# Performance work log

Measured on AMD Instinct MI355X. Metric: run time of the kernel, lower is better.

Reference implementation:

```python
import jax, jax.numpy as jnp
import numpy as np

IN_CH, OUT_CH = 32, 32
MODES1, MODES2 = 16, 16
B, H, W = 16, 256, 256


def setup_inputs() -> dict:
    key = jax.random.key(0)
    k1, k2, k3 = jax.random.split(key, 3)
    scale = 1.0 / (IN_CH * OUT_CH)
    x = jax.random.normal(k1, (B, IN_CH, H, W), dtype=jnp.float32)
    # weights stored as real view of complex: [..., 2] = (real, imag)
    w1 = scale * jax.random.uniform(k2, (IN_CH, OUT_CH, MODES1, MODES2, 2), dtype=jnp.float32)
    w2 = scale * jax.random.uniform(k3, (IN_CH, OUT_CH, MODES1, MODES2, 2), dtype=jnp.float32)
    return {"x": x, "w1": w1, "w2": w2}


def reference(x, w1, w2):
    m1, m2 = MODES1, MODES2
    b, _, h, w = x.shape
    x_ft = jnp.fft.rfft2(x, axes=(-2, -1))  # [B, in_ch, H, W//2+1] complex
    c1 = w1[..., 0] + 1j * w1[..., 1]       # [in_ch, out_ch, m1, m2]
    c2 = w2[..., 0] + 1j * w2[..., 1]
    o1 = jnp.einsum('bixy,ioxy->boxy', x_ft[:, :, :m1, :m2], c1)
    o2 = jnp.einsum('bixy,ioxy->boxy', x_ft[:, :, -m1:, :m2], c2)
    out_ft = jnp.zeros((b, c1.shape[1], h, w // 2 + 1), dtype=x_ft.dtype)
    out_ft = out_ft.at[:, :, :m1, :m2].set(o1)
    out_ft = out_ft.at[:, :, -m1:, :m2].set(o2)
    return jnp.fft.irfft2(out_ft, s=(h, w), axes=(-2, -1))
```

## Files before the change

### kernel.cpp

```cpp
#include <hip/hip_runtime.h>
#include <math.h>

#define BB 16
#define CC 32
#define HH 256
#define WW 256
#define NIMG (BB * CC)

typedef _Float16 f16;
typedef __attribute__((ext_vector_type(8))) _Float16 f16x8;
typedef __attribute__((ext_vector_type(4))) float f32x4;

constexpr float TWO_PI_OVER_256 = 6.28318530717958647692f / 256.0f;

#define N_TWF 8192
#define N_ACOL 32768
#define N_AINV 16384
#define N_BINV 8192

static __device__ __forceinline__ f32x4 mfma3(f16x8 ah, f16x8 al, f16x8 bh,
                                              f16x8 bl, f32x4 c) {
  c = __builtin_amdgcn_mfma_f32_16x16x32_f16(ah, bh, c, 0, 0, 0);
  c = __builtin_amdgcn_mfma_f32_16x16x32_f16(ah, bl, c, 0, 0, 0);
  c = __builtin_amdgcn_mfma_f32_16x16x32_f16(al, bh, c, 0, 0, 0);
  return c;
}

static __device__ __forceinline__ void split16(float v, f16* hi, f16* lo) {
  f16 h_ = (f16)v;
  *hi = h_;
  *lo = (f16)(v - (float)h_);
}

__global__ __launch_bounds__(256) void k_tw(f16* __restrict__ fb) {
  const int id = blockIdx.x * 256 + threadIdx.x;
  f16* twf_hi = fb;
  f16* twf_lo = twf_hi + N_TWF;
  f16* acol_hi = twf_lo + N_TWF;
  f16* acol_lo = acol_hi + N_ACOL;
  f16* ainv_hi = acol_lo + N_ACOL;
  f16* ainv_lo = ainv_hi + N_AINV;
  f16* binv_hi = ainv_lo + N_AINV;
  f16* binv_lo = binv_hi + N_BINV;

  float v;
  f16 *dh, *dl;
  if (id < N_TWF) {
    int idx = id;
    int j = idx & 7, lane = (idx >> 3) & 63, ks = (idx >> 9) & 7,
        nt = (idx >> 12) & 1;
    int col = nt * 16 + (lane & 15);
    int w = ks * 32 + ((lane >> 4) << 3) + j;
    int kx = col >> 1, ri = col & 1;
    int ph = (kx * w) & 255;
    float s, c;
    sincosf(TWO_PI_OVER_256 * (float)ph, &s, &c);
    v = ri ? -s : c;
    dh = twf_hi + idx;
    dl = twf_lo + idx;
  } else if (id < N_TWF + N_ACOL) {
    int idx = id - N_TWF;
    int j = idx & 7, lane = (idx >> 3) & 63, ks = (idx >> 9) & 7,
        mt = (idx >> 12) & 3, half = (idx >> 14) & 1;
    int row = mt * 16 + (lane & 15);
    int k = ks * 32 + ((lane >> 4) << 3) + j;
    int h = half * 128 + (k >> 1);
    int rj = k & 1;
    int zr = (row < 32) ? row : row - 32;
    int ky = (zr < 16) ? zr : 224 + zr;
    int ph = (ky * h) & 255;
    float s, c;
    sincosf(TWO_PI_OVER_256 * (float)ph, &s, &c);
    if (row < 32)
      v = rj ? s : c;
    else
      v = rj ? c : -s;
    dh = acol_hi + idx;
    dl = acol_lo + idx;
  } else if (id < N_TWF + N_ACOL + N_AINV) {
    int idx = id - N_TWF - N_ACOL;
    int j = idx & 7, lane = (idx >> 3) & 63, ks = (idx >> 9) & 1,
        mt = (idx >> 10) & 15;
    int h = mt * 16 + (lane & 15);
    int k = ks * 32 + ((lane >> 4) << 3) + j;
    int zr = k >> 1, rj = k & 1;
    int ky = (zr < 16) ? zr : 224 + zr;
    int ph = (ky * h) & 255;
    float s, c;
    sincosf(TWO_PI_OVER_256 * (float)ph, &s, &c);
    v = rj ? s : c;
    dh = ainv_hi + idx;
    dl = ainv_lo + idx;
  } else {
    int idx = id - N_TWF - N_ACOL - N_AINV;
    int j = idx & 7, lane = (idx >> 3) & 63, nt = (idx >> 9) & 15;
    int w = nt * 16 + (lane & 15);
    int k = ((lane >> 4) << 3) + j;
    int kx = k >> 1, ri = k & 1;
    int ph = (kx * w) & 255;
    float s, c;
    sincosf(TWO_PI_OVER_256 * (float)ph, &s, &c);
    float scale = ((kx == 0) ? 1.0f : 2.0f) / 65536.0f;
    v = ri ? -scale * s : scale * c;
    dh = binv_hi + idx;
    dl = binv_lo + idx;
  }
  f16 hi, lo;
  split16(v, &hi, &lo);
  *dh = hi;
  *dl = lo;
}

__global__ __launch_bounds__(256) void k_fwd(const float* __restrict__ x,
                                             const f16* __restrict__ twf_hi,
                                             const f16* __restrict__ twf_lo,
                                             const f16* __restrict__ acol_hi,
                                             const f16* __restrict__ acol_lo,
                                             float* __restrict__ Zp) {
  __shared__ __align__(16) float xs[2][32][256];
  __shared__ __align__(16) f16 Yc_hi[16 * 256];
  __shared__ __align__(16) f16 Yc_lo[16 * 256];
  const int t = threadIdx.x, lane = t & 63, wid = t >> 6;
  const int l15 = lane & 15, kgrp = lane >> 4;
  const int img = blockIdx.x >> 1;
  const int half = blockIdx.x & 1;
  const float* xim = x + (size_t)img * (HH * WW) + half * 128 * WW;
  const int mt = wid >> 1;
  const int nt = wid & 1;

  f16x8 tbh[8], tbl[8];
#pragma unroll
  for (int ks = 0; ks < 8; ++ks) {
    const int bo = ((nt * 8 + ks) * 64 + lane) * 8;
    tbh[ks] = *(const f16x8*)(twf_hi + bo);
    tbl[ks] = *(const f16x8*)(twf_lo + bo);
  }
  asm volatile("" ::: "memory");

  auto STAGE = [&](int c, int b) {
#pragma unroll
    for (int i = 0; i < 8; ++i) {
      const int row = wid * 8 + i;
      const int go = (lane * 16) ^ ((row & 7) << 4);
      __builtin_amdgcn_global_load_lds(
          (const __attribute__((address_space(1))) void*)(xim +
                                                          (c * 32 + row) * WW +
                                                          (go >> 2)),
          (__attribute__((address_space(3))) void*)&xs[b][row][0], 16, 0, 0);
    }
  };

  STAGE(0, 0);
  STAGE(1, 1);

#pragma unroll
  for (int c = 0; c < 4; ++c) {
    if (c == 3)
      asm volatile("s_waitcnt vmcnt(0)" ::: "memory");
    else
      asm volatile("s_waitcnt vmcnt(8)" ::: "memory");
    __builtin_amdgcn_s_barrier();
    {
      const int row = mt * 16 + l15;
      const char* rb = (const char*)&xs[c & 1][row][0];
      const int swz = (row & 7) << 4;
      f32x4 acc = {0.f, 0.f, 0.f, 0.f};
#pragma unroll
      for (int ks = 0; ks < 8; ++ks) {
        const int off = 128 * ks + 32 * kgrp;
        float4 a0 = *(const float4*)(rb + (off ^ swz));
        float4 a1 = *(const float4*)(rb + ((off + 16) ^ swz));
        float vv[8] = {a0.x, a0.y, a0.z, a0.w, a1.x, a1.y, a1.z, a1.w};
        f16x8 ah, al;
#pragma unroll
        for (int e = 0; e < 8; ++e) {
          f16 h_ = (f16)vv[e];
          ah[e] = h_;
          al[e] = (f16)(vv[e] - (float)h_);
        }
        acc = mfma3(ah, al, tbh[ks], tbl[ks], acc);
      }
      const int n = nt * 16 + l15;
      const int kx = n >> 1, ri = n & 1;
      char* yh = (char*)Yc_hi + kx * 512;
      char* yl = (char*)Yc_lo + kx * 512;
      const int kswz = (kx & 7) << 4;
#pragma unroll
      for (int jj = 0; jj < 4; ++jj) {
        const int hl = c * 32 + mt * 16 + kgrp * 4 + jj;
        const int boff = (4 * hl + 2 * ri) ^ kswz;
        float v = acc[jj];
        f16 hv = (f16)v;
        *(f16*)(yh + boff) = hv;
        *(f16*)(yl + boff) = (f16)(v - (float)hv);
      }
    }
    asm volatile("s_waitcnt lgkmcnt(0)" ::: "memory");
    __builtin_amdgcn_s_barrier();
    if (c < 2) STAGE(c + 2, c & 1);
  }

  f32x4 zacc = {0.f, 0.f, 0.f, 0.f};
  const int kswz2 = (l15 & 7) << 4;
  const char* ybh = (const char*)Yc_hi + l15 * 512;
  const char* ybl = (const char*)Yc_lo + l15 * 512;
#pragma unroll
  for (int ks = 0; ks < 8; ++ks) {
    const int ao = ((((half * 4 + wid) * 8) + ks) * 64 + lane) * 8;
    f16x8 a_h = *(const f16x8*)(acol_hi + ao);
    f16x8 a_l = *(const f16x8*)(acol_lo + ao);
    const int boff = (64 * ks + 16 * kgrp) ^ kswz2;
    f16x8 b_h = *(const f16x8*)(ybh + boff);
    f16x8 b_l = *(const f16x8*)(ybl + boff);
    zacc = mfma3(a_h, a_l, b_h, b_l, zacc);
  }
  float* zp = Zp + ((size_t)img * 2 + half) * 1024;
#pragma unroll
  for (int jj = 0; jj < 4; ++jj) {
    const int row = wid * 16 + kgrp * 4 + jj;
    zp[row * 16 + l15] = zacc[jj];
  }
}

__global__ __launch_bounds__(256) void k_mix(const float* __restrict__ Zp,
                                             const float* __restrict__ w1,
                                             const float* __restrict__ w2,
                                             float* __restrict__ O) {
  __shared__ float zsr[CC][16];
  __shared__ float zsi[CC][16];
  const int t = threadIdx.x;
  const int b = blockIdx.x >> 5;
  const int zr = blockIdx.x & 31;
  const int kyi = zr & 15;
  const float* wsrc = (zr < 16) ? w1 : w2;
  {
    const int i = t >> 3, reim = (t >> 2) & 1, f4 = t & 3;
    const float* base = Zp + ((size_t)(b * CC + i) * 2) * 1024 + reim * 512 +
                        zr * 16 + f4 * 4;
    float4 a = *(const float4*)(base);
    float4 c = *(const float4*)(base + 1024);
    float4 s = make_float4(a.x + c.x, a.y + c.y, a.z + c.z, a.w + c.w);
    if (reim == 0)
      *(float4*)&zsr[i][f4 * 4] = s;
    else
      *(float4*)&zsi[i][f4 * 4] = s;
  }
  __syncthreads();
  const int kx = t & 15;
  const int oc0 = t >> 4;
  const float2* cp = (const float2*)wsrc;
#pragma unroll
  for (int pass = 0; pass < 2; ++pass) {
    const int oc = oc0 + pass * 16;
    float acc_r = 0.f, acc_i = 0.f;
#pragma unroll 4
    for (int i = 0; i < CC; ++i) {
      float zre = zsr[i][kx];
      float zim = zsi[i][kx];
      float2 cv = cp[(size_t)(i * CC + oc) * 256 + kyi * 16 + kx];
      acc_r += zre * cv.x - zim * cv.y;
      acc_i += zre * cv.y + zim * cv.x;
    }
    float2* dst = (float2*)O + (size_t)(b * CC + oc) * 512 + zr * 16 + kx;
    *dst = make_float2(acc_r, acc_i);
  }
}

__global__ __launch_bounds__(256) void k_inv(const float* __restrict__ O,
                                             const f16* __restrict__ ainv_hi,
                                             const f16* __restrict__ ainv_lo,
                                             const f16* __restrict__ binv_hi,
                                             const f16* __restrict__ binv_lo,
                                             float* __restrict__ out) {
  __shared__ float Olds[1024];
  __shared__ __align__(16) f16 Bf_hi[2048], Bf_lo[2048];
  __shared__ __align__(16) f16 T_hi[128 * 40], T_lo[128 * 40];
  const int t = threadIdx.x, lane = t & 63, wid = t >> 6;
  const int l15 = lane & 15, kgrp = lane >> 4;
  const int img = blockIdx.x >> 1;
  const int half = blockIdx.x & 1;
  {
    float4 v = ((const float4*)(O + (size_t)img * 1024))[t];
    *(float4*)&Olds[t * 4] = v;
  }
  __syncthreads();
#pragma unroll
  for (int e = 0; e < 8; ++e) {
    const int idx = e * 256 + t;
    const int nt = idx >> 10, ks = (idx >> 9) & 1, ln = (idx >> 3) & 63,
              j = idx & 7;
    const int k = ks * 32 + ((ln >> 4) << 3) + j;
    const int n = nt * 16 + (ln & 15);
    const int zr = k >> 1, rj = k & 1, kx = n >> 1, ri = n & 1;
    const float Or = Olds[(zr * 16 + kx) * 2];
    const float Oi = Olds[(zr * 16 + kx) * 2 + 1];
    const float v = (rj == 0) ? (ri == 0 ? Or : Oi) : (ri == 0 ? -Oi : Or);
    f16 hv = (f16)v;
    Bf_hi[idx] = hv;
    Bf_lo[idx] = (f16)(v - (float)hv);
  }
  __syncthreads();
#pragma unroll
  for (int mm = 0; mm < 2; ++mm) {
    const int mtl = wid * 2 + mm;
    const int mt = half * 8 + mtl;
    f32x4 acc0 = {0.f, 0.f, 0.f, 0.f}, acc1 = {0.f, 0.f, 0.f, 0.f};
#pragma unroll
    for (int ks = 0; ks < 2; ++ks) {
      const int ao = ((mt * 2 + ks) * 64 + lane) * 8;
      f16x8 a_h = *(const f16x8*)(ainv_hi + ao);
      f16x8 a_l = *(const f16x8*)(ainv_lo + ao);
      const int bo0 = ((0 * 2 + ks) * 64 + lane) * 8;
      const int bo1 = ((1 * 2 + ks) * 64 + lane) * 8;
      f16x8 b0h = *(const f16x8*)(Bf_hi + bo0);
      f16x8 b0l = *(const f16x8*)(Bf_lo + bo0);
      f16x8 b1h = *(const f16x8*)(Bf_hi + bo1);
      f16x8 b1l = *(const f16x8*)(Bf_lo + bo1);
      acc0 = mfma3(a_h, a_l, b0h, b0l, acc0);
      acc1 = mfma3(a_h, a_l, b1h, b1l, acc1);
    }
#pragma unroll
    for (int nt = 0; nt < 2; ++nt) {
#pragma unroll
      for (int jj = 0; jj < 4; ++jj) {
        const int hl = mtl * 16 + kgrp * 4 + jj;
        const int n = nt * 16 + l15;
        float v = (nt == 0) ? acc0[jj] : acc1[jj];
        f16 hv = (f16)v;
        T_hi[hl * 40 + n] = hv;
        T_lo[hl * 40 + n] = (f16)(v - (float)hv);
      }
    }
  }
  __syncthreads();
  float* op = out + (size_t)img * (HH * WW) + (size_t)half * 128 * WW;
#pragma unroll
  for (int mm = 0; mm < 2; ++mm) {
    const int mtl = wid * 2 + mm;
    const int ao = (mtl * 16 + l15) * 40 + kgrp * 8;
    f16x8 a_h = *(const f16x8*)(T_hi + ao);
    f16x8 a_l = *(const f16x8*)(T_lo + ao);
#pragma unroll 4
    for (int nt = 0; nt < 16; ++nt) {
      const int bo = (nt * 64 + lane) * 8;
      f16x8 b_h = *(const f16x8*)(binv_hi + bo);
      f16x8 b_l = *(const f16x8*)(binv_lo + bo);
      f32x4 acc = {0.f, 0.f, 0.f, 0.f};
      acc = mfma3(a_h, a_l, b_h, b_l, acc);
#pragma unroll
      for (int jj = 0; jj < 4; ++jj) {
        const int hl = mtl * 16 + kgrp * 4 + jj;
        op[(size_t)hl * WW + nt * 16 + l15] = acc[jj];
      }
    }
  }
}

extern "C" void kernel_launch(void* const* d_in, const int* in_sizes, int n_in,
                              void* d_out, int out_size, void* d_ws,
                              size_t ws_size, hipStream_t stream) {
  const float* x = (const float*)d_in[0];
  const float* w1 = (const float*)d_in[1];
  const float* w2 = (const float*)d_in[2];
  float* out = (float*)d_out;

  f16* fb = (f16*)d_ws;
  f16* twf_hi = fb;
  f16* twf_lo = twf_hi + N_TWF;
  f16* acol_hi = twf_lo + N_TWF;
  f16* acol_lo = acol_hi + N_ACOL;
  f16* ainv_hi = acol_lo + N_ACOL;
  f16* ainv_lo = ainv_hi + N_AINV;
  f16* binv_hi = ainv_lo + N_AINV;
  f16* binv_lo = binv_hi + N_BINV;
  float* Zp = (float*)(binv_lo + N_BINV);
  float* O = Zp + (size_t)NIMG * 2048;

  k_tw<<<dim3(256), dim3(256), 0, stream>>>(fb);
  k_fwd<<<dim3(NIMG * 2), dim3(256), 0, stream>>>(x, twf_hi, twf_lo, acol_hi,
                                                  acol_lo, Zp);
  k_mix<<<dim3(BB * 32), dim3(256), 0, stream>>>(Zp, w1, w2, O);
  k_inv<<<dim3(NIMG * 2), dim3(256), 0, stream>>>(O, ainv_hi, ainv_lo, binv_hi,
                                                  binv_lo, out);
}
```

Before: 77.34 us.

## Process full image per k_inv block and stage inverse twiddles in LDS

Each k_inv block now handles a whole 256x256 output image instead of half of it, which halves the grid and removes the duplicated O loading and column-pass matmul work per image. The binv hi/lo twiddle matrices are prefetched into registers at kernel start and written into LDS once the Bf buffer (which they overlay) is free, so the row-pass MFMAs read B operands from LDS instead of global memory. The cost is a much larger LDS footprint (about 76 KB per block), which limits blocks per CU, and fewer blocks overall.

New measurement: 83.94 us. +8.5%, slower.

```diff
diff --git a/kernel.cpp b/kernel.cpp
--- a/kernel.cpp
+++ b/kernel.cpp
@@ -272,13 +272,23 @@
                                              const f16* __restrict__ binv_hi,
                                              const f16* __restrict__ binv_lo,
                                              float* __restrict__ out) {
-  __shared__ float Olds[1024];
-  __shared__ __align__(16) f16 Bf_hi[2048], Bf_lo[2048];
-  __shared__ __align__(16) f16 T_hi[128 * 40], T_lo[128 * 40];
+  __shared__ __align__(16) char raw[77824];
+  float* Olds = (float*)raw;
+  f16* T_hi = (f16*)(raw + 4096);
+  f16* T_lo = (f16*)(raw + 24576);
+  f16* Bf_hi = (f16*)(raw + 45056);
+  f16* Bf_lo = (f16*)(raw + 49152);
+  f16* binv_lds = (f16*)(raw + 45056);
   const int t = threadIdx.x, lane = t & 63, wid = t >> 6;
   const int l15 = lane & 15, kgrp = lane >> 4;
-  const int img = blockIdx.x >> 1;
-  const int half = blockIdx.x & 1;
+  const int img = blockIdx.x;
+
+  float4 breg[8];
+  {
+    const float4* bsrc = (const float4*)binv_hi;
+#pragma unroll
+    for (int k = 0; k < 8; ++k) breg[k] = bsrc[t + k * 256];
+  }
   {
     float4 v = ((const float4*)(O + (size_t)img * 1024))[t];
     *(float4*)&Olds[t * 4] = v;
@@ -301,9 +311,8 @@
   }
   __syncthreads();
 #pragma unroll
-  for (int mm = 0; mm < 2; ++mm) {
-    const int mtl = wid * 2 + mm;
-    const int mt = half * 8 + mtl;
+  for (int mm = 0; mm < 4; ++mm) {
+    const int mt = wid * 4 + mm;
     f32x4 acc0 = {0.f, 0.f, 0.f, 0.f}, acc1 = {0.f, 0.f, 0.f, 0.f};
 #pragma unroll
     for (int ks = 0; ks < 2; ++ks) {
@@ -323,34 +332,40 @@
     for (int nt = 0; nt < 2; ++nt) {
 #pragma unroll
       for (int jj = 0; jj < 4; ++jj) {
-        const int hl = mtl * 16 + kgrp * 4 + jj;
+        const int h = mt * 16 + kgrp * 4 + jj;
         const int n = nt * 16 + l15;
         float v = (nt == 0) ? acc0[jj] : acc1[jj];
         f16 hv = (f16)v;
-        T_hi[hl * 40 + n] = hv;
-        T_lo[hl * 40 + n] = (f16)(v - (float)hv);
+        T_hi[h * 40 + n] = hv;
+        T_lo[h * 40 + n] = (f16)(v - (float)hv);
       }
     }
   }
   __syncthreads();
-  float* op = out + (size_t)img * (HH * WW) + (size_t)half * 128 * WW;
-#pragma unroll
-  for (int mm = 0; mm < 2; ++mm) {
-    const int mtl = wid * 2 + mm;
-    const int ao = (mtl * 16 + l15) * 40 + kgrp * 8;
+  {
+    float4* bl = (float4*)binv_lds;
+#pragma unroll
+    for (int k = 0; k < 8; ++k) bl[t + k * 256] = breg[k];
+  }
+  __syncthreads();
+  float* op = out + (size_t)img * (HH * WW);
+#pragma unroll
+  for (int mm = 0; mm < 4; ++mm) {
+    const int mt = wid * 4 + mm;
+    const int ao = (mt * 16 + l15) * 40 + kgrp * 8;
     f16x8 a_h = *(const f16x8*)(T_hi + ao);
     f16x8 a_l = *(const f16x8*)(T_lo + ao);
 #pragma unroll 4
     for (int nt = 0; nt < 16; ++nt) {
       const int bo = (nt * 64 + lane) * 8;
-      f16x8 b_h = *(const f16x8*)(binv_hi + bo);
-      f16x8 b_l = *(const f16x8*)(binv_lo + bo);
+      f16x8 b_h = *(const f16x8*)(binv_lds + bo);
+      f16x8 b_l = *(const f16x8*)(binv_lds + 8192 + bo);
       f32x4 acc = {0.f, 0.f, 0.f, 0.f};
       acc = mfma3(a_h, a_l, b_h, b_l, acc);
 #pragma unroll
       for (int jj = 0; jj < 4; ++jj) {
-        const int hl = mtl * 16 + kgrp * 4 + jj;
-        op[(size_t)hl * WW + nt * 16 + l15] = acc[jj];
+        const int h = mt * 16 + kgrp * 4 + jj;
+        op[(size_t)h * WW + nt * 16 + l15] = acc[jj];
       }
     }
   }
@@ -380,6 +395,6 @@
   k_fwd<<<dim3(NIMG * 2), dim3(256), 0, stream>>>(x, twf_hi, twf_lo, acol_hi,
                                                   acol_lo, Zp);
   k_mix<<<dim3(BB * 32), dim3(256), 0, stream>>>(Zp, w1, w2, O);
-  k_inv<<<dim3(NIMG * 2), dim3(256), 0, stream>>>(O, ainv_hi, ainv_lo, binv_hi,
-                                                  binv_lo, out);
-}
+  k_inv<<<dim3(NIMG), dim3(256), 0, stream>>>(O, ainv_hi, ainv_lo, binv_hi,
+                                              binv_lo, out);
+}
```

## Fuse all stages into one persistent cooperative kernel with grid syncs

Applied to the files above, without the earlier changes.

Replaces the four separate launches (twiddle table build, forward DFT, spectral mixing, inverse DFT) with a single cooperative persistent kernel. Blocks loop over tasks and separate the stages with grid.sync(). The intent is to remove per-launch overhead and the idle gaps between kernels. In exchange, grid size is capped by occupancy (at most 512 blocks). Each block now handles both image halves serially in the forward stage, which may lower parallelism, and grid barriers add their own cost.

Result: slower. 196.2 us (+153.6%).

```diff
diff --git a/kernel.cpp b/kernel.cpp
--- a/kernel.cpp
+++ b/kernel.cpp
@@ -1,5 +1,8 @@
 #include <hip/hip_runtime.h>
+#include <hip/hip_cooperative_groups.h>
 #include <math.h>
+
+namespace cg = cooperative_groups;
 
 #define BB 16
 #define CC 32
@@ -32,8 +35,7 @@
   *lo = (f16)(v - (float)h_);
 }
 
-__global__ __launch_bounds__(256) void k_tw(f16* __restrict__ fb) {
-  const int id = blockIdx.x * 256 + threadIdx.x;
+static __device__ __forceinline__ void build_table(int id, f16* __restrict__ fb) {
   f16* twf_hi = fb;
   f16* twf_lo = twf_hi + N_TWF;
   f16* acol_hi = twf_lo + N_TWF;
@@ -111,6 +113,271 @@
   *dl = lo;
 }
 
+__global__ __launch_bounds__(256) void k_all(const float* __restrict__ x,
+                                             const float* __restrict__ w1,
+                                             const float* __restrict__ w2,
+                                             float* __restrict__ out,
+                                             f16* __restrict__ fb,
+                                             float* __restrict__ Zp,
+                                             float* __restrict__ Og) {
+  __shared__ __align__(16) char smem[81920];
+  cg::grid_group grid = cg::this_grid();
+  const int t = threadIdx.x, lane = t & 63, wid = t >> 6;
+  const int l15 = lane & 15, kgrp = lane >> 4;
+  const int bid = blockIdx.x, gD = gridDim.x;
+
+  const f16* twf_hi = fb;
+  const f16* twf_lo = twf_hi + N_TWF;
+  const f16* acol_hi = twf_lo + N_TWF;
+  const f16* acol_lo = acol_hi + N_ACOL;
+  const f16* ainv_hi = acol_lo + N_ACOL;
+  const f16* ainv_lo = ainv_hi + N_AINV;
+  const f16* binv_hi = ainv_lo + N_AINV;
+  const f16* binv_lo = binv_hi + N_BINV;
+
+  for (int task = bid; task < 256; task += gD) build_table(task * 256 + t, fb);
+  grid.sync();
+
+  {
+    float* xs = (float*)smem;
+    char* ychb = smem + 65536;
+    char* yclb = smem + 73728;
+    const int mt = wid >> 1;
+    const int nt = wid & 1;
+    f16x8 tbh[8], tbl[8];
+#pragma unroll
+    for (int ks = 0; ks < 8; ++ks) {
+      const int bo = ((nt * 8 + ks) * 64 + lane) * 8;
+      tbh[ks] = *(const f16x8*)(twf_hi + bo);
+      tbl[ks] = *(const f16x8*)(twf_lo + bo);
+    }
+    asm volatile("" ::: "memory");
+
+    for (int task = bid; task < NIMG; task += gD) {
+      const float* xim0 = x + (size_t)task * (HH * WW);
+      for (int half = 0; half < 2; ++half) {
+        const float* xim = xim0 + half * 128 * WW;
+        auto STAGE = [&](int c, int b) {
+#pragma unroll
+          for (int i = 0; i < 8; ++i) {
+            const int row = wid * 8 + i;
+            const int go = (lane * 16) ^ ((row & 7) << 4);
+            __builtin_amdgcn_global_load_lds(
+                (const __attribute__((address_space(1))) void*)(xim + (c * 32 + row) * WW + (go >> 2)),
+                (__attribute__((address_space(3))) void*)(xs + b * 8192 + row * 256),
+                16, 0, 0);
+          }
+        };
+        STAGE(0, 0);
+        STAGE(1, 1);
+#pragma unroll
+        for (int c = 0; c < 4; ++c) {
+          if (c == 3)
+            asm volatile("s_waitcnt vmcnt(0)" ::: "memory");
+          else
+            asm volatile("s_waitcnt vmcnt(8)" ::: "memory");
+          __builtin_amdgcn_s_barrier();
+          {
+            const int row = mt * 16 + l15;
+            const char* rb = (const char*)(xs + (c & 1) * 8192 + row * 256);
+            const int swz = (row & 7) << 4;
+            f32x4 acc = {0.f, 0.f, 0.f, 0.f};
+#pragma unroll
+            for (int ks = 0; ks < 8; ++ks) {
+              const int off = 128 * ks + 32 * kgrp;
+              float4 a0 = *(const float4*)(rb + (off ^ swz));
+              float4 a1 = *(const float4*)(rb + ((off + 16) ^ swz));
+              float vv[8] = {a0.x, a0.y, a0.z, a0.w, a1.x, a1.y, a1.z, a1.w};
+              f16x8 ah, al;
+#pragma unroll
+              for (int e = 0; e < 8; ++e) {
+                f16 h_ = (f16)vv[e];
+                ah[e] = h_;
+                al[e] = (f16)(vv[e] - (float)h_);
+              }
+              acc = mfma3(ah, al, tbh[ks], tbl[ks], acc);
+            }
+            const int n = nt * 16 + l15;
+            const int kx = n >> 1, ri = n & 1;
+            char* yh = ychb + kx * 512;
+            char* yl = yclb + kx * 512;
+            const int kswz = (kx & 7) << 4;
+#pragma unroll
+            for (int jj = 0; jj < 4; ++jj) {
+              const int hl = c * 32 + mt * 16 + kgrp * 4 + jj;
+              const int boff = (4 * hl + 2 * ri) ^ kswz;
+              float v = acc[jj];
+              f16 hv = (f16)v;
+              *(f16*)(yh + boff) = hv;
+              *(f16*)(yl + boff) = (f16)(v - (float)hv);
+            }
+          }
+          asm volatile("s_waitcnt lgkmcnt(0)" ::: "memory");
+          __builtin_amdgcn_s_barrier();
+          if (c < 2) STAGE(c + 2, c & 1);
+        }
+        f32x4 zacc = {0.f, 0.f, 0.f, 0.f};
+        const int kswz2 = (l15 & 7) << 4;
+        const char* ybh = ychb + l15 * 512;
+        const char* ybl = yclb + l15 * 512;
+#pragma unroll
+        for (int ks = 0; ks < 8; ++ks) {
+          const int ao = ((((half * 4 + wid) * 8) + ks) * 64 + lane) * 8;
+          f16x8 a_h = *(const f16x8*)(acol_hi + ao);
+          f16x8 a_l = *(const f16x8*)(acol_lo + ao);
+          const int boff = (64 * ks + 16 * kgrp) ^ kswz2;
+          f16x8 b_h = *(const f16x8*)(ybh + boff);
+          f16x8 b_l = *(const f16x8*)(ybl + boff);
+          zacc = mfma3(a_h, a_l, b_h, b_l, zacc);
+        }
+        float* zp = Zp + ((size_t)task * 2 + half) * 1024;
+#pragma unroll
+        for (int jj = 0; jj < 4; ++jj) {
+          const int row = wid * 16 + kgrp * 4 + jj;
+          zp[row * 16 + l15] = zacc[jj];
+        }
+      }
+    }
+  }
+  grid.sync();
+
+  {
+    float* zsr = (float*)smem;
+    float* zsi = (float*)(smem + 2048);
+    for (int task = bid; task < 512; task += gD) {
+      const int b = task >> 5;
+      const int zr = task & 31;
+      const int kyi = zr & 15;
+      const float* wsrc = (zr < 16) ? w1 : w2;
+      {
+        const int i = t >> 3, reim = (t >> 2) & 1, f4 = t & 3;
+        const float* base = Zp + ((size_t)(b * CC + i) * 2) * 1024 +
+                            reim * 512 + zr * 16 + f4 * 4;
+        float4 a = *(const float4*)(base);
+        float4 c = *(const float4*)(base + 1024);
+        float4 s = make_float4(a.x + c.x, a.y + c.y, a.z + c.z, a.w + c.w);
+        if (reim == 0)
+          *(float4*)&zsr[i * 16 + f4 * 4] = s;
+        else
+          *(float4*)&zsi[i * 16 + f4 * 4] = s;
+      }
+      __syncthreads();
+      const int kx = t & 15;
+      const int oc0 = t >> 4;
+      const float2* cp = (const float2*)wsrc;
+#pragma unroll
+      for (int pass = 0; pass < 2; ++pass) {
+        const int oc = oc0 + pass * 16;
+        float acc_r = 0.f, acc_i = 0.f;
+#pragma unroll 4
+        for (int i = 0; i < CC; ++i) {
+          float zre = zsr[i * 16 + kx];
+          float zim = zsi[i * 16 + kx];
+          float2 cv = cp[(size_t)(i * CC + oc) * 256 + kyi * 16 + kx];
+          acc_r += zre * cv.x - zim * cv.y;
+          acc_i += zre * cv.y + zim * cv.x;
+        }
+        float2* dst = (float2*)Og + (size_t)(b * CC + oc) * 512 + zr * 16 + kx;
+        *dst = make_float2(acc_r, acc_i);
+      }
+      __syncthreads();
+    }
+  }
+  grid.sync();
+
+  {
+    float* Olds = (float*)smem;
+    f16* T_hi = (f16*)(smem + 4096);
+    f16* T_lo = (f16*)(smem + 14336);
+    f16* Bf_hi = (f16*)(smem + 24576);
+    f16* Bf_lo = (f16*)(smem + 28672);
+    for (int task = bid; task < NIMG; task += gD) {
+      {
+        float4 v = ((const float4*)(Og + (size_t)task * 1024))[t];
+        *(float4*)&Olds[t * 4] = v;
+      }
+      __syncthreads();
+#pragma unroll
+      for (int e = 0; e < 8; ++e) {
+        const int idx = e * 256 + t;
+        const int nt = idx >> 10, ks = (idx >> 9) & 1, ln = (idx >> 3) & 63,
+                  j = idx & 7;
+        const int k = ks * 32 + ((ln >> 4) << 3) + j;
+        const int n = nt * 16 + (ln & 15);
+        const int zr = k >> 1, rj = k & 1, kx = n >> 1, ri = n & 1;
+        const float Or = Olds[(zr * 16 + kx) * 2];
+        const float Oi = Olds[(zr * 16 + kx) * 2 + 1];
+        const float v = (rj == 0) ? (ri == 0 ? Or : Oi) : (ri == 0 ? -Oi : Or);
+        f16 hv = (f16)v;
+        Bf_hi[idx] = hv;
+        Bf_lo[idx] = (f16)(v - (float)hv);
+      }
+      __syncthreads();
+      for (int half = 0; half < 2; ++half) {
+#pragma unroll
+        for (int mm = 0; mm < 2; ++mm) {
+          const int mtl = wid * 2 + mm;
+          const int mt = half * 8 + mtl;
+          f32x4 acc0 = {0.f, 0.f, 0.f, 0.f}, acc1 = {0.f, 0.f, 0.f, 0.f};
+#pragma unroll
+          for (int ks = 0; ks < 2; ++ks) {
+            const int ao = ((mt * 2 + ks) * 64 + lane) * 8;
+            f16x8 a_h = *(const f16x8*)(ainv_hi + ao);
+            f16x8 a_l = *(const f16x8*)(ainv_lo + ao);
+            const int bo0 = ((0 * 2 + ks) * 64 + lane) * 8;
+            const int bo1 = ((1 * 2 + ks) * 64 + lane) * 8;
+            f16x8 b0h = *(const f16x8*)(Bf_hi + bo0);
+            f16x8 b0l = *(const f16x8*)(Bf_lo + bo0);
+            f16x8 b1h = *(const f16x8*)(Bf_hi + bo1);
+            f16x8 b1l = *(const f16x8*)(Bf_lo + bo1);
+            acc0 = mfma3(a_h, a_l, b0h, b0l, acc0);
+            acc1 = mfma3(a_h, a_l, b1h, b1l, acc1);
+          }
+#pragma unroll
+          for (int nt = 0; nt < 2; ++nt) {
+#pragma unroll
+            for (int jj = 0; jj < 4; ++jj) {
+              const int hl = mtl * 16 + kgrp * 4 + jj;
+              const int n = nt * 16 + l15;
+              float v = (nt == 0) ? acc0[jj] : acc1[jj];
+              f16 hv = (f16)v;
+              T_hi[hl * 40 + n] = hv;
+              T_lo[hl * 40 + n] = (f16)(v - (float)hv);
+            }
+          }
+        }
+        __syncthreads();
+        float* op = out + (size_t)task * (HH * WW) + (size_t)half * 128 * WW;
+#pragma unroll
+        for (int mm = 0; mm < 2; ++mm) {
+          const int mtl = wid * 2 + mm;
+          const int ao = (mtl * 16 + l15) * 40 + kgrp * 8;
+          f16x8 a_h = *(const f16x8*)(T_hi + ao);
+          f16x8 a_l = *(const f16x8*)(T_lo + ao);
+#pragma unroll 4
+          for (int nt = 0; nt < 16; ++nt) {
+            const int bo = (nt * 64 + lane) * 8;
+            f16x8 b_h = *(const f16x8*)(binv_hi + bo);
+            f16x8 b_l = *(const f16x8*)(binv_lo + bo);
+            f32x4 acc = {0.f, 0.f, 0.f, 0.f};
+            acc = mfma3(a_h, a_l, b_h, b_l, acc);
+#pragma unroll
+            for (int jj = 0; jj < 4; ++jj) {
+              const int hl = mtl * 16 + kgrp * 4 + jj;
+              op[(size_t)hl * WW + nt * 16 + l15] = acc[jj];
+            }
+          }
+        }
+        __syncthreads();
+      }
+    }
+  }
+}
+
+__global__ __launch_bounds__(256) void k_tw(f16* __restrict__ fb) {
+  build_table(blockIdx.x * 256 + threadIdx.x, fb);
+}
+
 __global__ __launch_bounds__(256) void k_fwd(const float* __restrict__ x,
                                              const f16* __restrict__ twf_hi,
                                              const f16* __restrict__ twf_lo,
@@ -143,9 +410,7 @@
       const int row = wid * 8 + i;
       const int go = (lane * 16) ^ ((row & 7) << 4);
       __builtin_amdgcn_global_load_lds(
-          (const __attribute__((address_space(1))) void*)(xim +
-                                                          (c * 32 + row) * WW +
-                                                          (go >> 2)),
+          (const __attribute__((address_space(1))) void*)(xim + (c * 32 + row) * WW + (go >> 2)),
           (__attribute__((address_space(3))) void*)&xs[b][row][0], 16, 0, 0);
     }
   };
@@ -376,10 +641,24 @@
   float* Zp = (float*)(binv_lo + N_BINV);
   float* O = Zp + (size_t)NIMG * 2048;
 
-  k_tw<<<dim3(256), dim3(256), 0, stream>>>(fb);
-  k_fwd<<<dim3(NIMG * 2), dim3(256), 0, stream>>>(x, twf_hi, twf_lo, acol_hi,
-                                                  acol_lo, Zp);
-  k_mix<<<dim3(BB * 32), dim3(256), 0, stream>>>(Zp, w1, w2, O);
-  k_inv<<<dim3(NIMG * 2), dim3(256), 0, stream>>>(O, ainv_hi, ainv_lo, binv_hi,
-                                                  binv_lo, out);
-}
+  int maxb = 0;
+  hipError_t qerr =
+      hipOccupancyMaxActiveBlocksPerMultiprocessor(&maxb, k_all, 256, 0);
+  int grid = 512;
+  if (qerr == hipSuccess && maxb >= 1) {
+    int cap = maxb * 256;
+    if (cap < grid) grid = cap;
+  }
+  void* args[] = {(void*)&x, (void*)&w1, (void*)&w2, (void*)&out,
+                  (void*)&fb, (void*)&Zp, (void*)&O};
+  hipError_t lerr = hipLaunchCooperativeKernel((void*)k_all, dim3(grid),
+                                               dim3(256), args, 0, stream);
+  if (lerr != hipSuccess) {
+    k_tw<<<dim3(256), dim3(256), 0, stream>>>(fb);
+    k_fwd<<<dim3(NIMG * 2), dim3(256), 0, stream>>>(x, twf_hi, twf_lo, acol_hi,
+                                                    acol_lo, Zp);
+    k_mix<<<dim3(BB * 32), dim3(256), 0, stream>>>(Zp, w1, w2, O);
+    k_inv<<<dim3(NIMG * 2), dim3(256), 0, stream>>>(O, ainv_hi, ainv_lo,
+                                                    binv_hi, binv_lo, out);
+  }
+}
```
